# Optimization experiments

Measured on AMD Instinct MI355X. Metric: run time of the kernel, lower is better.

## Reference

```python
import jax, jax.numpy as jnp
import numpy as np

START_DISP = 0
DISP_NUM = 192
B, C, H, W = 2, 1, 384, 1248


def setup_inputs() -> dict:
    key = jax.random.key(0)
    k1, k2 = jax.random.split(key)
    left = jax.random.normal(k1, (B, C, H, W), dtype=jnp.float32)
    right = jax.random.normal(k2, (B, C, H, W), dtype=jnp.float32)
    return {"left_img": left, "right_img": right}


def _gen_cost(left, right):
    # left, right: [B,1,H,W] -> cost: [B,D,H,W]
    Wd = left.shape[-1]
    l = left[:, 0]   # [B,H,W]
    r = right[:, 0]  # [B,H,W]
    disp = jnp.arange(START_DISP, START_DISP + DISP_NUM)          # [D]
    idx = jnp.arange(Wd)[None, :] - disp[:, None]                 # [D,W] source col in right
    valid = (idx >= 0) & (idx < Wd)                               # region written by the torch loop
    r_shift = jnp.take(r, jnp.clip(idx, 0, Wd - 1), axis=-1)      # [B,H,D,W]
    r_shift = jnp.moveaxis(r_shift, 2, 1)                         # [B,D,H,W]
    cost = jnp.where(valid[None, :, None, :], l[:, None, :, :] * r_shift,
                     jnp.zeros((), dtype=l.dtype))
    return cost


def _regress(cost):
    disp_values = jnp.arange(START_DISP, START_DISP + DISP_NUM,
                             dtype=cost.dtype).reshape(1, -1, 1, 1)
    return jnp.sum(cost * disp_values, axis=1)  # [B,H,W]


def reference(left_img, right_img):
    cost = _gen_cost(left_img, right_img)
    return _regress(cost)
```

## Files before the change

### kernel.cpp

```cpp
#include <hip/hip_runtime.h>


#define WID 1248
#define DISP 192
#define SEG 312
#define THREADS 256
#define NROWS 768

__global__ __launch_bounds__(THREADS) void stereo_scan_kernel(
    const float* __restrict__ left,
    const float* __restrict__ right,
    float* __restrict__ out)
{
    __shared__ float Ps[520];
    __shared__ float Qs[520];
    __shared__ float wsS[4], wsQ[4];

    const int bid = blockIdx.x;
    const int row = bid >> 2;
    const int seg = bid & 3;
    const int wstart = seg * SEG;
    const long base = (long)row * WID;
    const int tid = threadIdx.x;
    const int lane = tid & 63;
    const int wv = tid >> 6;

    const int i0 = 2 * tid;
    const int j0 = wstart - (DISP - 1) + i0;
    float e0 = (j0     >= 0 && j0     < WID) ? right[base + j0]     : 0.0f;
    float e1 = (j0 + 1 >= 0 && j0 + 1 < WID) ? right[base + j0 + 1] : 0.0f;

    float s = e0 + e1;
    float q = fmaf((float)i0, e0, (float)(i0 + 1) * e1);
    const float ls = s, lq = q;

    #pragma unroll
    for (int d = 1; d < 64; d <<= 1) {
        float ts = __shfl_up(s, (unsigned)d, 64);
        float tq = __shfl_up(q, (unsigned)d, 64);
        if (lane >= d) { s += ts; q += tq; }
    }
    if (lane == 63) { wsS[wv] = s; wsQ[wv] = q; }
    __syncthreads();

    float offS = 0.0f, offQ = 0.0f;
    if (wv > 0) { offS += wsS[0]; offQ += wsQ[0]; }
    if (wv > 1) { offS += wsS[1]; offQ += wsQ[1]; }
    if (wv > 2) { offS += wsS[2]; offQ += wsQ[2]; }

    const float exS = offS + s - ls;
    const float exQ = offQ + q - lq;
    Ps[i0]     = exS;
    Ps[i0 + 1] = exS + e0;
    Qs[i0]     = exQ;
    Qs[i0 + 1] = fmaf((float)i0, e0, exQ);
    __syncthreads();

    {
        const int t = tid;
        const float A  = Ps[t + DISP] - Ps[t];
        const float Qw = Qs[t + DISP] - Qs[t];
        const float S  = fmaf((float)(t + DISP - 1), A, -Qw);
        const int w = wstart + t;
        out[base + w] = left[base + w] * S;
    }
    if (tid < SEG - THREADS) {
        const int t = THREADS + tid;
        const float A  = Ps[t + DISP] - Ps[t];
        const float Qw = Qs[t + DISP] - Qs[t];
        const float S  = fmaf((float)(t + DISP - 1), A, -Qw);
        const int w = wstart + t;
        out[base + w] = left[base + w] * S;
    }
}

extern "C" void kernel_launch(void* const* d_in, const int* in_sizes, int n_in,
                              void* d_out, int out_size, void* d_ws, size_t ws_size,
                              hipStream_t stream) {
    const float* left  = (const float*)d_in[0];
    const float* right = (const float*)d_in[1];
    float* out = (float*)d_out;
    stereo_scan_kernel<<<dim3(NROWS * 4), dim3(THREADS), 0, stream>>>(left, right, out);
}
```

Measured before the change: 61.47 us.

## Process a whole row per block with float4 loads and skewed shared prefix arrays

Replaces the four-segment-per-row decomposition with one block per image row of 320 threads. Each thread loads four contiguous right and left values as float4 and does a local scan before the wave-level shuffle scan. This removes the redundant halo reloads of right pixels that overlapped across segments. Shared-memory prefix arrays are padded with a skew to reduce bank conflicts. The trade-off is four times fewer blocks (768), which lowers parallelism, and some idle threads in the last wave.

```diff
diff --git a/kernel.cpp b/kernel.cpp
--- a/kernel.cpp
+++ b/kernel.cpp
@@ -1,76 +1,104 @@
 #include <hip/hip_runtime.h>
 
 
-#define WID 1248
-#define DISP 192
-#define SEG 312
-#define THREADS 256
+#define WID   1248
+#define DISP  192
+#define THREADS 320
 #define NROWS 768
 
-__global__ __launch_bounds__(THREADS) void stereo_scan_kernel(
+#define SKEW(i) ((i) + ((i) >> 5))
+
+__global__ __launch_bounds__(THREADS) void stereo_row_kernel(
     const float* __restrict__ left,
     const float* __restrict__ right,
     float* __restrict__ out)
 {
-    __shared__ float Ps[520];
-    __shared__ float Qs[520];
-    __shared__ float wsS[4], wsQ[4];
+    __shared__ float Ps[1320];
+    __shared__ float Qs[1320];
+    __shared__ float wsS[5], wsQ[5];
 
-    const int bid = blockIdx.x;
-    const int row = bid >> 2;
-    const int seg = bid & 3;
-    const int wstart = seg * SEG;
+    const int  row  = blockIdx.x;
     const long base = (long)row * WID;
-    const int tid = threadIdx.x;
-    const int lane = tid & 63;
-    const int wv = tid >> 6;
+    const int  tid  = threadIdx.x;
+    const int  lane = tid & 63;
+    const int  wv   = tid >> 6;
+    const int  i0   = tid << 2;
+    const bool active = (i0 < WID);
 
-    const int i0 = 2 * tid;
-    const int j0 = wstart - (DISP - 1) + i0;
-    float e0 = (j0     >= 0 && j0     < WID) ? right[base + j0]     : 0.0f;
-    float e1 = (j0 + 1 >= 0 && j0 + 1 < WID) ? right[base + j0 + 1] : 0.0f;
+    float e0 = 0.f, e1 = 0.f, e2 = 0.f, e3 = 0.f;
+    float l0 = 0.f, l1 = 0.f, l2 = 0.f, l3 = 0.f;
+    if (active) {
+        const float4 ev = *reinterpret_cast<const float4*>(right + base + i0);
+        const float4 lv = *reinterpret_cast<const float4*>(left  + base + i0);
+        e0 = ev.x; e1 = ev.y; e2 = ev.z; e3 = ev.w;
+        l0 = lv.x; l1 = lv.y; l2 = lv.z; l3 = lv.w;
+    }
 
-    float s = e0 + e1;
-    float q = fmaf((float)i0, e0, (float)(i0 + 1) * e1);
-    const float ls = s, lq = q;
+    const float fi0 = (float)i0;
+    const float ts  = (e0 + e1) + (e2 + e3);
+    const float tq  = fmaf(fi0,        e0,
+                      fmaf(fi0 + 1.f,  e1,
+                      fmaf(fi0 + 2.f,  e2, (fi0 + 3.f) * e3)));
 
+    float s = ts, q = tq;
     #pragma unroll
     for (int d = 1; d < 64; d <<= 1) {
-        float ts = __shfl_up(s, (unsigned)d, 64);
-        float tq = __shfl_up(q, (unsigned)d, 64);
-        if (lane >= d) { s += ts; q += tq; }
+        const float us = __shfl_up(s, (unsigned)d, 64);
+        const float uq = __shfl_up(q, (unsigned)d, 64);
+        if (lane >= d) { s += us; q += uq; }
     }
     if (lane == 63) { wsS[wv] = s; wsQ[wv] = q; }
     __syncthreads();
 
-    float offS = 0.0f, offQ = 0.0f;
-    if (wv > 0) { offS += wsS[0]; offQ += wsQ[0]; }
-    if (wv > 1) { offS += wsS[1]; offQ += wsQ[1]; }
-    if (wv > 2) { offS += wsS[2]; offQ += wsQ[2]; }
+    float offS = 0.f, offQ = 0.f;
+    #pragma unroll
+    for (int w2 = 0; w2 < 4; ++w2) {
+        if (wv > w2) { offS += wsS[w2]; offQ += wsQ[w2]; }
+    }
 
-    const float exS = offS + s - ls;
-    const float exQ = offQ + q - lq;
-    Ps[i0]     = exS;
-    Ps[i0 + 1] = exS + e0;
-    Qs[i0]     = exQ;
-    Qs[i0 + 1] = fmaf((float)i0, e0, exQ);
+    float p  = offS + (s - ts);
+    float qv = offQ + (q - tq);
+
+    Ps[SKEW(i0)]     = p;   Qs[SKEW(i0)]     = qv;
+    p += e0;                qv = fmaf(fi0,       e0, qv);
+    Ps[SKEW(i0 + 1)] = p;   Qs[SKEW(i0 + 1)] = qv;
+    p += e1;                qv = fmaf(fi0 + 1.f, e1, qv);
+    Ps[SKEW(i0 + 2)] = p;   Qs[SKEW(i0 + 2)] = qv;
+    p += e2;                qv = fmaf(fi0 + 2.f, e2, qv);
+    Ps[SKEW(i0 + 3)] = p;   Qs[SKEW(i0 + 3)] = qv;
     __syncthreads();
 
-    {
-        const int t = tid;
-        const float A  = Ps[t + DISP] - Ps[t];
-        const float Qw = Qs[t + DISP] - Qs[t];
-        const float S  = fmaf((float)(t + DISP - 1), A, -Qw);
-        const int w = wstart + t;
-        out[base + w] = left[base + w] * S;
-    }
-    if (tid < SEG - THREADS) {
-        const int t = THREADS + tid;
-        const float A  = Ps[t + DISP] - Ps[t];
-        const float Qw = Qs[t + DISP] - Qs[t];
-        const float S  = fmaf((float)(t + DISP - 1), A, -Qw);
-        const int w = wstart + t;
-        out[base + w] = left[base + w] * S;
+    if (active) {
+        float r0, r1, r2, r3;
+        {
+            const int w  = i0;
+            const int lo = (w > DISP - 1) ? (w - (DISP - 1)) : 0;
+            const float A  = Ps[SKEW(w + 1)] - Ps[SKEW(lo)];
+            const float Qw = Qs[SKEW(w + 1)] - Qs[SKEW(lo)];
+            r0 = l0 * fmaf((float)w, A, -Qw);
+        }
+        {
+            const int w  = i0 + 1;
+            const int lo = (w > DISP - 1) ? (w - (DISP - 1)) : 0;
+            const float A  = Ps[SKEW(w + 1)] - Ps[SKEW(lo)];
+            const float Qw = Qs[SKEW(w + 1)] - Qs[SKEW(lo)];
+            r1 = l1 * fmaf((float)w, A, -Qw);
+        }
+        {
+            const int w  = i0 + 2;
+            const int lo = (w > DISP - 1) ? (w - (DISP - 1)) : 0;
+            const float A  = Ps[SKEW(w + 1)] - Ps[SKEW(lo)];
+            const float Qw = Qs[SKEW(w + 1)] - Qs[SKEW(lo)];
+            r2 = l2 * fmaf((float)w, A, -Qw);
+        }
+        {
+            const int w  = i0 + 3;
+            const int lo = (w > DISP - 1) ? (w - (DISP - 1)) : 0;
+            const float A  = Ps[SKEW(w + 1)] - Ps[SKEW(lo)];
+            const float Qw = Qs[SKEW(w + 1)] - Qs[SKEW(lo)];
+            r3 = l3 * fmaf((float)w, A, -Qw);
+        }
+        *reinterpret_cast<float4*>(out + base + i0) = make_float4(r0, r1, r2, r3);
     }
 }
 
@@ -80,5 +108,5 @@
     const float* left  = (const float*)d_in[0];
     const float* right = (const float*)d_in[1];
     float* out = (float*)d_out;
-    stereo_scan_kernel<<<dim3(NROWS * 4), dim3(THREADS), 0, stream>>>(left, right, out);
+    stereo_row_kernel<<<dim3(NROWS), dim3(THREADS), 0, stream>>>(left, right, out);
 }
```

Result: faster. 59.69 us (-2.9%).
